# Optimization experiments

Hardware: AMD Instinct MI355X
Metric: run time of the kernel (lower is better)

## Reference

```python
import jax, jax.numpy as jnp
import numpy as np


def _elu(x):
    return jnp.where(x > 0, x, jnp.expm1(x))


def setup_inputs() -> dict:
    key = jax.random.key(0)
    ks = jax.random.split(key, 12)
    B, T, E, A, S, H, L = 1024, 50, 1024, 6, 200, 200, 30
    g = lambda k, shape, s=0.05: (jax.random.normal(k, shape, jnp.float32) * s)
    return {
        "action": jax.random.normal(ks[0], (B, T, A), jnp.float32),
        "embed": jax.random.normal(ks[1], (B, T, E), jnp.float32),
        "noise": jax.random.normal(ks[2], (B, T, L), jnp.float32),
        # GRUCell params (PyTorch gate order r,z,n), stored as [in, 3S]
        "W_ih": g(ks[3], (A + E, 3 * S)),
        "W_hh": g(ks[4], (S, 3 * S)),
        "b_ih": jnp.zeros((3 * S,), jnp.float32),
        "b_hh": jnp.zeros((3 * S,), jnp.float32),
        # fc_prior: Linear(S,H) -> ELU -> Linear(H, 2L)
        "Wp1": g(ks[5], (S, H)), "bp1": jnp.zeros((H,), jnp.float32),
        "Wp2": g(ks[6], (H, 2 * L)), "bp2": jnp.zeros((2 * L,), jnp.float32),
        # fc_posterior: Linear(S+E,H) -> ELU -> Linear(H, 2L)
        "Wq1": g(ks[7], (S + E, H)), "bq1": jnp.zeros((H,), jnp.float32),
        "Wq2": g(ks[8], (H, 2 * L)), "bq2": jnp.zeros((2 * L,), jnp.float32),
    }


def reference(action, embed, noise, W_ih, W_hh, b_ih, b_hh,
              Wp1, bp1, Wp2, bp2, Wq1, bq1, Wq2, bq2):
    B = action.shape[0]
    S = W_hh.shape[0]

    def gru(x, h):
        # PyTorch GRUCell: gates r, z, n
        gi = x @ W_ih + b_ih
        gh = h @ W_hh + b_hh
        i_r, i_z, i_n = jnp.split(gi, 3, -1)
        h_r, h_z, h_n = jnp.split(gh, 3, -1)
        r = jax.nn.sigmoid(i_r + h_r)
        z = jax.nn.sigmoid(i_z + h_z)
        n = jnp.tanh(i_n + r * h_n)
        return (1.0 - z) * n + z * h

    def step(deter, inp):
        a_t, e_t, eps_t = inp  # [B,A], [B,E], [B,L]
        deter = gru(jnp.concatenate([a_t, e_t], -1), deter)
        pm, ps = jnp.split(_elu(deter @ Wp1 + bp1) @ Wp2 + bp2, 2, -1)
        qm, qs = jnp.split(
            _elu(jnp.concatenate([deter, e_t], -1) @ Wq1 + bq1) @ Wq2 + bq2, 2, -1)
        ps = jax.nn.softplus(ps) + 0.1
        qs = jax.nn.softplus(qs) + 0.1
        stoch = qm + qs * eps_t  # posterior rsample
        return deter, (deter, stoch, pm, ps, qm, qs)

    deter0 = jnp.zeros((B, S), action.dtype)
    xs = (jnp.swapaxes(action, 0, 1),
          jnp.swapaxes(embed, 0, 1),
          jnp.swapaxes(noise, 0, 1))
    _, outs = jax.lax.scan(step, deter0, xs)
    # [T,B,*] -> [B,T,*]; pack (deter, stoch, prior mean/std, post mean/std)
    outs = [jnp.swapaxes(o, 0, 1) for o in outs]
    return jnp.concatenate(outs, -1)  # [B, T, S + 5L]
```

## Files before the change

### kernel.cpp

```cpp
#include <hip/hip_runtime.h>
#include <hip/hip_bf16.h>
#include <cstdint>


typedef __attribute__((ext_vector_type(8))) short   short8;
typedef __attribute__((ext_vector_type(8))) __bf16  bf16x8;
typedef __attribute__((ext_vector_type(4))) float   f32x4;

__device__ __forceinline__ float bf2f(unsigned short u) {
    unsigned int v = ((unsigned int)u) << 16;
    return __builtin_bit_cast(float, v);
}
__device__ __forceinline__ unsigned short f2bf(float f) {
    unsigned int v = __builtin_bit_cast(unsigned int, f);
    v = v + 0x7FFFu + ((v >> 16) & 1u);
    return (unsigned short)(v >> 16);
}
__device__ __forceinline__ float softplusf(float x) {
    return (x > 20.f) ? x : log1pf(__expf(x));
}
__device__ __forceinline__ void gload_lds16(const void* g, void* l) {
    __builtin_amdgcn_global_load_lds(
        (const __attribute__((address_space(1))) void*)g,
        (__attribute__((address_space(3))) void*)l, 16, 0, 0);
}

#define OFF_BPACK 81920000
#define OFF_WHH   83558400
#define OFF_WPQ1  83837952
#define OFF_WPQ2  84024320


__global__ __launch_bounds__(256) void pack_kernel(
    const float* __restrict__ W_ih, const float* __restrict__ W_hh,
    const float* __restrict__ Wp1,  const float* __restrict__ Wq1,
    const float* __restrict__ Wp2,  const float* __restrict__ Wq2,
    unsigned short* __restrict__ Bpack, unsigned short* __restrict__ Whh_p,
    unsigned short* __restrict__ Wpq1,  unsigned short* __restrict__ Wpq2)
{
    int e = blockIdx.x * 256 + threadIdx.x;
    if (e < 819200) {
        const int j = e & 7, l = (e >> 3) & 63;
        const int nt = (e >> 9) % 50, kk = e / (512 * 50);
        const int k = kk * 32 + (l >> 4) * 8 + j;
        const int c = nt * 16 + (l & 15);
        Bpack[e] = f2bf((c < 600) ? W_ih[(6 + k) * 600 + c]
                                  : Wq1[(200 + k) * 200 + (c - 600)]);
        return;
    }
    e -= 819200;
    if (e < 139776) {
        const int j = e & 7, l = (e >> 3) & 63;
        const int nt = (e >> 9) % 39, kk = e / (512 * 39);
        const int k = kk * 32 + (l >> 4) * 8 + j;
        const int g = nt / 13, st = nt % 13;
        const int c = st * 16 + (l & 15);
        Whh_p[e] = (k < 200 && c < 200) ? f2bf(W_hh[k * 600 + g * 200 + c]) : (unsigned short)0;
        return;
    }
    e -= 139776;
    if (e < 93184) {
        const int j = e & 7, l = (e >> 3) & 63;
        const int nt = (e >> 9) % 26, kk = e / (512 * 26);
        const int k = kk * 32 + (l >> 4) * 8 + j;
        unsigned short v = 0;
        if (nt < 13) { const int c = nt * 16 + (l & 15);        if (k < 200 && c < 200) v = f2bf(Wp1[k * 200 + c]); }
        else         { const int c = (nt - 13) * 16 + (l & 15); if (k < 200 && c < 200) v = f2bf(Wq1[k * 200 + c]); }
        Wpq1[e] = v;
        return;
    }
    e -= 93184;
    if (e < 28672) {
        const int j = e & 7, l = (e >> 3) & 63;
        const int nt = (e >> 9) % 8, kk = e / (512 * 8);
        const int k = kk * 32 + (l >> 4) * 8 + j;
        unsigned short v = 0;
        if (nt < 4) { const int c = nt * 16 + (l & 15);       if (k < 200 && c < 60) v = f2bf(Wp2[k * 60 + c]); }
        else        { const int c = (nt - 4) * 16 + (l & 15); if (k < 200 && c < 60) v = f2bf(Wq2[k * 60 + c]); }
        Wpq2[e] = v;
    }
}

#define K1_BUF 13312
__global__ __launch_bounds__(256, 3) void k1_gi(
    const float* __restrict__ embed,
    const float* __restrict__ action,
    const float* __restrict__ W_ih,
    const float* __restrict__ b_ih,
    const float* __restrict__ bq1,
    const unsigned short* __restrict__ Bpack,
    unsigned short* __restrict__ GI)
{
    __shared__ short bufS[2][K1_BUF];

    const int tid = threadIdx.x;
    const int w = tid >> 6, l = tid & 63;
    const int lo = l & 15, hi = l >> 4;

    const int g    = (blockIdx.x & 7) * 250 + (blockIdx.x >> 3);
    const int mblk = g / 5;
    const int ng   = g - mblk * 5;
    const int rb   = mblk * 128;

    const char* sp[7]; int st[7]; int dof[7]; bool en[7];
#pragma unroll
    for (int i = 0; i < 7; ++i) {
        const int j = w + 4 * i;
        en[i] = (j < 26);
        const int jc = (j < 26) ? j : 25;
        if (jc < 10) {
            sp[i]  = (const char*)(Bpack + (size_t)(ng * 10 + jc) * 512 + l * 8);
            st[i]  = 50 * 512 * 2;
            dof[i] = jc * 512;
        } else {
            const int a = jc - 10, m = a >> 1, h = a & 1;
            sp[i]  = (const char*)(embed + (size_t)(rb + m * 16 + (l & 15)) * 1024
                                         + (l >> 4) * 8 + h * 4);
            st[i]  = 32 * 4;
            dof[i] = 5120 + a * 512;
        }
    }

    f32x4 acc[2][10];
#pragma unroll
    for (int m = 0; m < 2; ++m)
#pragma unroll
        for (int i = 0; i < 10; ++i) acc[m][i] = f32x4{0.f, 0.f, 0.f, 0.f};

#pragma unroll
    for (int i = 0; i < 7; ++i) if (en[i]) {
        gload_lds16(sp[i], &bufS[0][dof[i]]);
        sp[i] += st[i];
    }
    __syncthreads();

    int cur = 0;
    for (int kk = 0; kk < 32; ++kk) {
        const int nxt = cur ^ 1;
        if (kk < 31) {
#pragma unroll
            for (int i = 0; i < 7; ++i) if (en[i]) {
                gload_lds16(sp[i], &bufS[nxt][dof[i]]);
                sp[i] += st[i];
            }
        }

        const float* Af = (const float*)&bufS[cur][5120];
        bf16x8 af[2];
#pragma unroll
        for (int m = 0; m < 2; ++m) {
            const int ms = w * 2 + m;
            f32x4 v0 = *(const f32x4*)&Af[(ms * 2 + 0) * 256 + l * 4];
            f32x4 v1 = *(const f32x4*)&Af[(ms * 2 + 1) * 256 + l * 4];
            bf16x8 t;
#pragma unroll
            for (int q = 0; q < 4; ++q) { t[q] = (__bf16)v0[q]; t[4 + q] = (__bf16)v1[q]; }
            af[m] = t;
        }
#pragma unroll
        for (int i = 0; i < 10; ++i) {
            bf16x8 b = __builtin_bit_cast(bf16x8, *(const short8*)&bufS[cur][i * 512 + l * 8]);
            acc[0][i] = __builtin_amdgcn_mfma_f32_16x16x32_bf16(af[0], b, acc[0][i], 0, 0, 0);
            acc[1][i] = __builtin_amdgcn_mfma_f32_16x16x32_bf16(af[1], b, acc[1][i], 0, 0, 0);
        }
        __syncthreads();
        cur = nxt;
    }

#pragma unroll
    for (int m = 0; m < 2; ++m) {
        const int rbase = rb + (w * 2 + m) * 16 + hi * 4;
        float av[4][6];
#pragma unroll
        for (int r = 0; r < 4; ++r)
#pragma unroll
            for (int k = 0; k < 6; ++k) av[r][k] = action[(size_t)(rbase + r) * 6 + k];
#pragma unroll
        for (int i = 0; i < 10; ++i) {
            const int col = ng * 160 + i * 16 + lo;
            const float bias = (col < 600) ? b_ih[col] : bq1[col - 600];
            float wa[6];
            if (col < 600) {
#pragma unroll
                for (int k = 0; k < 6; ++k) wa[k] = W_ih[k * 600 + col];
            }
#pragma unroll
            for (int r = 0; r < 4; ++r) {
                float v = acc[m][i][r] + bias;
                if (col < 600) {
#pragma unroll
                    for (int k = 0; k < 6; ++k) v += av[r][k] * wa[k];
                }
                GI[(size_t)(rbase + r) * 800 + col] = f2bf(v);
            }
        }
    }
}

#define HSTRB 232
#define GSTR  227

__global__ __launch_bounds__(512, 2) void k2_scan(
    unsigned short* __restrict__ GI,
    const unsigned short* __restrict__ Whh_p,
    const float* __restrict__ b_hh,
    float* __restrict__ out)
{
    __shared__ unsigned short hS[16 * HSTRB];
    __shared__ float gAll[3 * 16 * GSTR];
    __shared__ __align__(16) unsigned short GIbuf[2][12288];

    const int tid = threadIdx.x;
    const int w = tid >> 6, l = tid & 63;
    const int lo = l & 15, hi = l >> 4;
    const int r0 = blockIdx.x * 16;

    for (int i = tid; i < 16 * HSTRB; i += 512) hS[i] = 0;

    const int t0 = w * 5;
    const int ntl = (w == 7) ? 4 : 5;
    bf16x8 wf[5][7];
#pragma unroll
    for (int i = 0; i < 5; ++i)
#pragma unroll
        for (int kk = 0; kk < 7; ++kk)
            if (i < ntl)
                wf[i][kk] = __builtin_bit_cast(bf16x8,
                    *(const short8*)&Whh_p[((kk * 39 + (t0 + i)) * 64 + l) * 8]);

    int gOff[5];
#pragma unroll
    for (int i = 0; i < 5; ++i) {
        int nt = t0 + i; if (nt > 38) nt = 38;
        const int g = nt / 13, st = nt - g * 13;
        gOff[i] = (g * 16 + hi * 4) * GSTR + st * 16 + lo;
    }

    const char* srcB[3];
#pragma unroll
    for (int i = 0; i < 3; ++i) {
        int j = (i * 8 + w) * 64 + l;
        int rj = j / 75; int cj = j - rj * 75;
        if (rj > 15) { rj = 15; cj = 74; }
        srcB[i] = (const char*)GI + (size_t)(r0 + rj) * 50 * 1600 + (size_t)cj * 16;
    }

    const int c = tid & 255;
    const int rh = tid >> 8;
    const bool act = (c < 200);
    float bh0 = 0.f, bh1 = 0.f, bh2 = 0.f;
    if (act) { bh0 = b_hh[c]; bh1 = b_hh[200 + c]; bh2 = b_hh[400 + c]; }
    float h_reg[8] = {0.f, 0.f, 0.f, 0.f, 0.f, 0.f, 0.f, 0.f};

    {
#pragma unroll
        for (int i = 0; i < 3; ++i)
            gload_lds16(srcB[i], &GIbuf[0][(i * 8 + w) * 512]);
    }
    asm volatile("s_waitcnt lgkmcnt(0)" ::: "memory");
    __builtin_amdgcn_s_barrier();
    __builtin_amdgcn_sched_barrier(0);

    for (int t = 0; t < 50; ++t) {
        const int tn = (t < 49) ? t + 1 : 49;
        const int bsel = (t + 1) & 1;
#pragma unroll
        for (int i = 0; i < 3; ++i)
            gload_lds16(srcB[i] + (size_t)tn * 1600, &GIbuf[bsel][(i * 8 + w) * 512]);

        bf16x8 hf[7];
#pragma unroll
        for (int kk = 0; kk < 7; ++kk)
            hf[kk] = __builtin_bit_cast(bf16x8,
                *(const short8*)&hS[lo * HSTRB + kk * 32 + hi * 8]);
        f32x4 acc[5];
#pragma unroll
        for (int i = 0; i < 5; ++i) acc[i] = f32x4{0.f, 0.f, 0.f, 0.f};
#pragma unroll
        for (int i = 0; i < 5; ++i) if (i < ntl)
#pragma unroll
            for (int kk = 0; kk < 7; ++kk)
                acc[i] = __builtin_amdgcn_mfma_f32_16x16x32_bf16(hf[kk], wf[i][kk], acc[i], 0, 0, 0);

#pragma unroll
        for (int i = 0; i < 5; ++i) if (i < ntl)
#pragma unroll
            for (int r = 0; r < 4; ++r)
                gAll[gOff[i] + r * GSTR] = acc[i][r];

        asm volatile("s_waitcnt lgkmcnt(0)" ::: "memory");
        __builtin_amdgcn_s_barrier();
        __builtin_amdgcn_sched_barrier(0);
        asm volatile("s_waitcnt vmcnt(3)" ::: "memory");
        __builtin_amdgcn_sched_barrier(0);

        if (act) {
            const unsigned short* gib = &GIbuf[t & 1][0];
#pragma unroll
            for (int rr = 0; rr < 8; ++rr) {
                const int row = rh * 8 + rr;
                const float gi_r = bf2f(gib[row * 600 + c]);
                const float gi_z = bf2f(gib[row * 600 + 200 + c]);
                const float gi_n = bf2f(gib[row * 600 + 400 + c]);
                const float gr = gi_r + gAll[(0 * 16 + row) * GSTR + c] + bh0;
                const float gz = gi_z + gAll[(1 * 16 + row) * GSTR + c] + bh1;
                const float hn = gAll[(2 * 16 + row) * GSTR + c] + bh2;
                const float rs = __builtin_amdgcn_rcpf(1.f + __expf(-gr));
                const float zz = __builtin_amdgcn_rcpf(1.f + __expf(-gz));
                const float x  = gi_n + rs * hn;
                const float e2 = __expf(-2.f * fabsf(x));
                float th = (1.f - e2) * __builtin_amdgcn_rcpf(1.f + e2);
                th = __builtin_copysignf(th, x);
                const float h = (1.f - zz) * th + zz * h_reg[rr];
                h_reg[rr] = h;
                hS[row * HSTRB + c] = f2bf(h);
                const size_t bt = (size_t)((r0 + row) * 50 + t);
                out[bt * 350 + c] = h;
                GI[bt * 800 + c]  = f2bf(h);
            }
        }

        asm volatile("s_waitcnt lgkmcnt(0)" ::: "memory");
        __builtin_amdgcn_s_barrier();
        __builtin_amdgcn_sched_barrier(0);
    }
}

__global__ __launch_bounds__(256, 1) void k3_heads(
    const unsigned short* __restrict__ GI,
    const unsigned short* __restrict__ Wpq1,
    const unsigned short* __restrict__ Wpq2,
    const float* __restrict__ noise,
    const float* __restrict__ bp1,
    const float* __restrict__ bp2,
    const float* __restrict__ bq2,
    float* __restrict__ out)
{
    __shared__ unsigned short pq[2][16 * HSTRB];
    __shared__ float ost[16 * 128];

    const int tid = threadIdx.x;
    const int w = tid >> 6, l = tid & 63;
    const int lo = l & 15, hi = l >> 4;
    const int r0 = blockIdx.x * 16;

    {   unsigned short* p0 = &pq[0][0];
        for (int i = tid; i < 2 * 16 * HSTRB; i += 256) p0[i] = 0; }
    __syncthreads();

    bf16x8 af[7];
#pragma unroll
    for (int kk = 0; kk < 7; ++kk)
        af[kk] = __builtin_bit_cast(bf16x8,
            *(const short8*)&GI[(size_t)(r0 + lo) * 800 + kk * 32 + hi * 8]);

    const int h1s = (w < 2) ? 7 * w : 14 + 6 * (w - 2);
    const int h1n = (w < 2) ? 7 : 6;
    f32x4 a2[7];
#pragma unroll
    for (int i = 0; i < 7; ++i) a2[i] = f32x4{0.f, 0.f, 0.f, 0.f};
#pragma unroll
    for (int i = 0; i < 7; ++i) if (i < h1n) {
        const int nt = h1s + i;
#pragma unroll
        for (int kk = 0; kk < 7; ++kk) {
            bf16x8 b = __builtin_bit_cast(bf16x8,
                *(const short8*)&Wpq1[((kk * 26 + nt) * 64 + l) * 8]);
            a2[i] = __builtin_amdgcn_mfma_f32_16x16x32_bf16(af[kk], b, a2[i], 0, 0, 0);
        }
    }
#pragma unroll
    for (int i = 0; i < 7; ++i) if (i < h1n) {
        const int nt = h1s + i;
        const bool isq = (nt >= 13);
        const int c1 = (isq ? (nt - 13) : nt) * 16 + lo;
        if (c1 < 200) {
#pragma unroll
            for (int r = 0; r < 4; ++r) {
                const int row = hi * 4 + r;
                float v = a2[i][r];
                if (isq) v += bf2f(GI[(size_t)(r0 + row) * 800 + 600 + c1]);
                else     v += bp1[c1];
                v = (v > 0.f) ? v : expm1f(v);
                pq[isq ? 1 : 0][row * HSTRB + c1] = f2bf(v);
            }
        }
    }
    __syncthreads();

    const unsigned short* srcS = &pq[(w >= 2) ? 1 : 0][0];
    bf16x8 pf[7];
#pragma unroll
    for (int kk = 0; kk < 7; ++kk)
        pf[kk] = __builtin_bit_cast(bf16x8,
            *(const short8*)&srcS[lo * HSTRB + kk * 32 + hi * 8]);
    f32x4 a3[2];
    a3[0] = f32x4{0.f, 0.f, 0.f, 0.f};
    a3[1] = f32x4{0.f, 0.f, 0.f, 0.f};
#pragma unroll
    for (int i = 0; i < 2; ++i) {
        const int nt = ((w >= 2) ? 4 : 0) + (w & 1) * 2 + i;
#pragma unroll
        for (int kk = 0; kk < 7; ++kk) {
            bf16x8 b = __builtin_bit_cast(bf16x8,
                *(const short8*)&Wpq2[((kk * 8 + nt) * 64 + l) * 8]);
            a3[i] = __builtin_amdgcn_mfma_f32_16x16x32_bf16(pf[kk], b, a3[i], 0, 0, 0);
        }
    }
#pragma unroll
    for (int i = 0; i < 2; ++i) {
        const int nt = ((w >= 2) ? 4 : 0) + (w & 1) * 2 + i;
        const int cl = (nt & 3) * 16 + lo;
        if (cl < 60) {
            const float bb = (nt < 4) ? bp2[cl] : bq2[cl];
            const int obase = ((nt < 4) ? 0 : 64) + ((cl < 30) ? cl : (32 + cl - 30));
#pragma unroll
            for (int r = 0; r < 4; ++r)
                ost[(hi * 4 + r) * 128 + obase] = a3[i][r] + bb;
        }
    }
    __syncthreads();

    for (int idx = tid; idx < 16 * 150; idx += 256) {
        const int row = idx / 150;
        const int c = 200 + (idx - row * 150);
        const size_t bt = (size_t)(r0 + row);
        const float* o = &ost[row * 128];
        float v;
        if (c < 230) {
            const int j = c - 200;
            const float qs = softplusf(o[96 + j]) + 0.1f;
            v = o[64 + j] + qs * noise[bt * 30 + j];
        }
        else if (c < 260) v = o[c - 230];
        else if (c < 290) v = softplusf(o[32 + (c - 260)]) + 0.1f;
        else if (c < 320) v = o[64 + (c - 290)];
        else              v = softplusf(o[96 + (c - 320)]) + 0.1f;
        out[bt * 350 + c] = v;
    }
}

extern "C" void kernel_launch(void* const* d_in, const int* in_sizes, int n_in,
                              void* d_out, int out_size, void* d_ws, size_t ws_size,
                              hipStream_t stream)
{
    const float* action = (const float*)d_in[0];
    const float* embed  = (const float*)d_in[1];
    const float* noise  = (const float*)d_in[2];
    const float* W_ih   = (const float*)d_in[3];
    const float* W_hh   = (const float*)d_in[4];
    const float* b_ih   = (const float*)d_in[5];
    const float* b_hh   = (const float*)d_in[6];
    const float* Wp1    = (const float*)d_in[7];
    const float* bp1    = (const float*)d_in[8];
    const float* Wp2    = (const float*)d_in[9];
    const float* bp2    = (const float*)d_in[10];
    const float* Wq1    = (const float*)d_in[11];
    const float* bq1    = (const float*)d_in[12];
    const float* Wq2    = (const float*)d_in[13];
    const float* bq2    = (const float*)d_in[14];
    (void)in_sizes; (void)n_in; (void)out_size; (void)ws_size;

    char* ws = (char*)d_ws;
    unsigned short* GI    = (unsigned short*)(ws);
    unsigned short* Bpack = (unsigned short*)(ws + OFF_BPACK);
    unsigned short* Whh_p = (unsigned short*)(ws + OFF_WHH);
    unsigned short* Wpq1  = (unsigned short*)(ws + OFF_WPQ1);
    unsigned short* Wpq2  = (unsigned short*)(ws + OFF_WPQ2);
    float* outp = (float*)d_out;

    pack_kernel<<<4222, 256, 0, stream>>>(W_ih, W_hh, Wp1, Wq1, Wp2, Wq2,
                                          Bpack, Whh_p, Wpq1, Wpq2);
    k1_gi<<<2000, 256, 0, stream>>>(embed, action, W_ih, b_ih, bq1, Bpack, GI);
    k2_scan<<<64, 512, 0, stream>>>(GI, Whh_p, b_hh, outp);
    k3_heads<<<3200, 256, 0, stream>>>(GI, Wpq1, Wpq2, noise, bp1, bp2, bq2, outp);
}
```

Baseline: 419.5 us.

## Overlap next-tile global-to-LDS loads with MFMA via partial vmcnt waits

Replaces the full __syncthreads after issuing the next stage's global_load_lds with per-wave s_waitcnt vmcnt(N), so only the current buffer's loads must land before the barrier and the prefetch of the next buffer stays in flight during compute. It also changes the embed tile load pattern so each 8-lane group reads a contiguous 128-byte row segment, making global reads more coalesced, and adjusts the LDS A-fragment addressing to match. The hand-written waitcnt and barrier sequence depends on exact per-wave load counts and risks races if the compiler reorders memory operations.

Result: faster. 369.8 us (-11.9%).

```diff
diff --git a/kernel.cpp b/kernel.cpp
--- a/kernel.cpp
+++ b/kernel.cpp
@@ -81,7 +81,7 @@
     }
 }
 
-#define K1_BUF 13312
+#define K1_BYTES 26624
 __global__ __launch_bounds__(256, 3) void k1_gi(
     const float* __restrict__ embed,
     const float* __restrict__ action,
@@ -91,7 +91,7 @@
     const unsigned short* __restrict__ Bpack,
     unsigned short* __restrict__ GI)
 {
-    __shared__ short bufS[2][K1_BUF];
+    __shared__ char bufS[2][K1_BYTES];
 
     const int tid = threadIdx.x;
     const int w = tid >> 6, l = tid & 63;
@@ -102,22 +102,21 @@
     const int ng   = g - mblk * 5;
     const int rb   = mblk * 128;
 
-    const char* sp[7]; int st[7]; int dof[7]; bool en[7];
+    const char* sp[7]; int st[7]; int dof[7];
+    const int nch = (w < 2) ? 7 : 6;
 #pragma unroll
     for (int i = 0; i < 7; ++i) {
-        const int j = w + 4 * i;
-        en[i] = (j < 26);
-        const int jc = (j < 26) ? j : 25;
-        if (jc < 10) {
-            sp[i]  = (const char*)(Bpack + (size_t)(ng * 10 + jc) * 512 + l * 8);
-            st[i]  = 50 * 512 * 2;
-            dof[i] = jc * 512;
+        int j = w + 4 * i; if (j >= 26) j = 25;
+        if (j < 10) {
+            sp[i]  = (const char*)Bpack + (size_t)(ng * 10 + j) * 1024 + l * 16;
+            st[i]  = 50 * 1024;
+            dof[i] = j * 1024;
         } else {
-            const int a = jc - 10, m = a >> 1, h = a & 1;
-            sp[i]  = (const char*)(embed + (size_t)(rb + m * 16 + (l & 15)) * 1024
-                                         + (l >> 4) * 8 + h * 4);
-            st[i]  = 32 * 4;
-            dof[i] = 5120 + a * 512;
+            const int a = j - 10;
+            sp[i]  = (const char*)embed
+                   + (size_t)(rb + a * 8 + (l >> 3)) * 4096 + (l & 7) * 16;
+            st[i]  = 128;
+            dof[i] = 10240 + a * 1024;
         }
     }
 
@@ -128,30 +127,36 @@
         for (int i = 0; i < 10; ++i) acc[m][i] = f32x4{0.f, 0.f, 0.f, 0.f};
 
 #pragma unroll
-    for (int i = 0; i < 7; ++i) if (en[i]) {
+    for (int i = 0; i < 7; ++i) if (i < nch) {
         gload_lds16(sp[i], &bufS[0][dof[i]]);
         sp[i] += st[i];
     }
-    __syncthreads();
 
     int cur = 0;
     for (int kk = 0; kk < 32; ++kk) {
         const int nxt = cur ^ 1;
         if (kk < 31) {
 #pragma unroll
-            for (int i = 0; i < 7; ++i) if (en[i]) {
+            for (int i = 0; i < 7; ++i) if (i < nch) {
                 gload_lds16(sp[i], &bufS[nxt][dof[i]]);
                 sp[i] += st[i];
             }
-        }
-
-        const float* Af = (const float*)&bufS[cur][5120];
+            if (w < 2) asm volatile("s_waitcnt vmcnt(7)" ::: "memory");
+            else       asm volatile("s_waitcnt vmcnt(6)" ::: "memory");
+        } else {
+            asm volatile("s_waitcnt vmcnt(0)" ::: "memory");
+        }
+        __builtin_amdgcn_s_barrier();
+        __builtin_amdgcn_sched_barrier(0);
+
+        const float* Af = (const float*)&bufS[cur][10240];
         bf16x8 af[2];
 #pragma unroll
         for (int m = 0; m < 2; ++m) {
             const int ms = w * 2 + m;
-            f32x4 v0 = *(const f32x4*)&Af[(ms * 2 + 0) * 256 + l * 4];
-            f32x4 v1 = *(const f32x4*)&Af[(ms * 2 + 1) * 256 + l * 4];
+            const float* rp = Af + (ms * 16 + lo) * 32 + hi * 8;
+            f32x4 v0 = *(const f32x4*)rp;
+            f32x4 v1 = *(const f32x4*)(rp + 4);
             bf16x8 t;
 #pragma unroll
             for (int q = 0; q < 4; ++q) { t[q] = (__bf16)v0[q]; t[4 + q] = (__bf16)v1[q]; }
@@ -159,11 +164,15 @@
         }
 #pragma unroll
         for (int i = 0; i < 10; ++i) {
-            bf16x8 b = __builtin_bit_cast(bf16x8, *(const short8*)&bufS[cur][i * 512 + l * 8]);
+            bf16x8 b = __builtin_bit_cast(bf16x8,
+                *(const short8*)&bufS[cur][i * 1024 + l * 16]);
             acc[0][i] = __builtin_amdgcn_mfma_f32_16x16x32_bf16(af[0], b, acc[0][i], 0, 0, 0);
             acc[1][i] = __builtin_amdgcn_mfma_f32_16x16x32_bf16(af[1], b, acc[1][i], 0, 0, 0);
         }
-        __syncthreads();
+
+        asm volatile("s_waitcnt lgkmcnt(0)" ::: "memory");
+        __builtin_amdgcn_s_barrier();
+        __builtin_amdgcn_sched_barrier(0);
         cur = nxt;
     }
 
```
